# Kernel tuning notes

Measured on AMD Instinct MI355X. Metric: run time of the kernel, lower is better.

## Reference

```python
import jax
import jax.numpy as jnp
import numpy as np

SAMPLE_RATE = 22050
CUTOFF = 0.4 * SAMPLE_RATE  # 0.8 * (sample_rate * 0.5)
Q = 0.707  # torchaudio default


def _biquad_coeffs():
    # torchaudio.functional.lowpass_biquad coefficient formulas
    w0 = 2.0 * np.pi * CUTOFF / SAMPLE_RATE  # = 0.8*pi
    alpha = np.sin(w0) / (2.0 * Q)
    cosw = np.cos(w0)
    a0 = 1.0 + alpha
    b0 = (1.0 - cosw) / 2.0 / a0
    b1 = (1.0 - cosw) / a0
    b2 = b0
    a1 = -2.0 * cosw / a0
    a2 = (1.0 - alpha) / a0
    return np.float32(b0), np.float32(b1), np.float32(b2), np.float32(a1), np.float32(a2)


def setup_inputs() -> dict:
    key = jax.random.key(0)
    inputs = jax.random.normal(key, (64, 262144), dtype=jnp.float32)
    return {"inputs": inputs}


def reference(inputs):
    b0, b1, b2, a1, a2 = _biquad_coeffs()
    x = inputs  # [B, T]
    # FIR (numerator) part, fully parallel
    x1 = jnp.pad(x[:, :-1], ((0, 0), (1, 0)))
    x2 = jnp.pad(x[:, :-2], ((0, 0), (2, 0)))
    u = b0 * x + b1 * x1 + b2 * x2  # [B, T]

    # IIR (denominator) recurrence: y[t] = u[t] - a1*y[t-1] - a2*y[t-2]
    def step(carry, ut):
        y1, y2 = carry
        y = ut - a1 * y1 - a2 * y2
        return (y, y1), y

    z = jnp.zeros(x.shape[0], dtype=x.dtype)
    _, ys = jax.lax.scan(step, (z, z), u.T)  # scan over time, carry [B]
    # torchaudio lfilter clamps output to [-1, 1] by default
    return jnp.clip(ys.T, -1.0, 1.0)
```

## Files before the change

kernel.cpp:

```cpp
#include <hip/hip_runtime.h>
#include <math.h>

constexpr int T_LEN = 262144;
constexpr int CH    = 16;
constexpr int WARM  = 48;
constexpr int TPB   = 256;
constexpr int SEG   = TPB * CH;
constexpr int LTOT  = SEG + WARM;
constexpr int LSWZ  = LTOT + LTOT/16 + 4;
constexpr int BPR   = T_LEN / SEG;

__device__ __forceinline__ int swz(int i) { return i + (i >> 4); }

__global__ __launch_bounds__(TPB, 8) void lowpass_kernel(
    const float* __restrict__ x, float* __restrict__ out,
    float b0, float b1, float b2, float a1, float a2)
{
    __shared__ float lds[LSWZ];
    const int tid = threadIdx.x;
    const size_t rbase = (size_t)(blockIdx.x / BPR) * T_LEN;
    const int blk  = blockIdx.x % BPR;
    const int seg0 = blk * SEG;
    const float* __restrict__ xr = x   + rbase;
    float*       __restrict__ yr = out + rbase;

    for (int m = tid; m < LTOT / 4; m += TPB) {
        const int idx  = 4 * m;
        const int gpos = seg0 - WARM + idx;
        float4 v = make_float4(0.f, 0.f, 0.f, 0.f);
        if (gpos >= 0) v = *reinterpret_cast<const float4*>(xr + gpos);
        const int sb = swz(idx);
        lds[sb + 0] = v.x; lds[sb + 1] = v.y;
        lds[sb + 2] = v.z; lds[sb + 3] = v.w;
    }
    __syncthreads();

    float x1 = 0.f, x2 = 0.f, y1 = 0.f, y2 = 0.f;
    const int b = 17 * tid;
    float o[CH];
    #pragma unroll
    for (int t = 0; t < WARM; ++t) {
        const float xc = lds[b + t + (t >> 4)];
        const float u  = fmaf(b0, xc, fmaf(b1, x1, b2 * x2));
        const float y  = fmaf(-a1, y1, fmaf(-a2, y2, u));
        x2 = x1; x1 = xc; y2 = y1; y1 = y;
    }
    #pragma unroll
    for (int t = 0; t < CH; ++t) {
        const float xc = lds[b + 51 + t];
        const float u  = fmaf(b0, xc, fmaf(b1, x1, b2 * x2));
        const float y  = fmaf(-a1, y1, fmaf(-a2, y2, u));
        x2 = x1; x1 = xc; y2 = y1; y1 = y;
        o[t] = fminf(fmaxf(y, -1.f), 1.f);
    }
    __syncthreads();

    #pragma unroll
    for (int t = 0; t < CH; ++t) lds[b + 51 + t] = o[t];
    __syncthreads();

    for (int m = tid; m < SEG / 4; m += TPB) {
        const int sb = 51 + 4 * m + (m >> 2);
        float4 v = make_float4(lds[sb], lds[sb + 1], lds[sb + 2], lds[sb + 3]);
        *reinterpret_cast<float4*>(yr + seg0 + 4 * m) = v;
    }
}

extern "C" void kernel_launch(void* const* d_in, const int* in_sizes, int n_in,
                              void* d_out, int out_size, void* d_ws, size_t ws_size,
                              hipStream_t stream) {
    const float* x = (const float*)d_in[0];
    float* out = (float*)d_out;
    const int rows = in_sizes[0] / T_LEN;

    const double SR = 22050.0, CUT = 0.4 * SR, Q = 0.707;
    double w0 = 2.0 * M_PI * CUT / SR;
    double alpha = sin(w0) / (2.0 * Q);
    double cosw = cos(w0);
    double a0d = 1.0 + alpha;
    float b0 = (float)((1.0 - cosw) / 2.0 / a0d);
    float b1 = (float)((1.0 - cosw) / a0d);
    float b2 = b0;
    float a1 = (float)(-2.0 * cosw / a0d);
    float a2 = (float)((1.0 - alpha) / a0d);

    const int blocks = rows * BPR;
    lowpass_kernel<<<blocks, TPB, 0, stream>>>(x, out, b0, b1, b2, a1, a2);
}
```

Before: 30.35 us.

## Use XOR-swizzled LDS with float4 accesses and shorten warm-up window

Replaces the padded (i + i/16) shared-memory layout with an XOR swizzle, so global-to-LDS staging, per-thread chunk reads and output writes can all use 128-bit float4 LDS accesses. The per-thread warm-up window is cut from 48 to 24 samples, which reduces redundant recurrence work and staging size. The staging loops are unrolled and the launch-bounds occupancy hint is lowered from 8 to 6. The shorter warm-up relies on the filter's impulse response decaying within 24 samples, which risks accuracy at segment boundaries.

```diff
diff --git a/kernel.cpp b/kernel.cpp
--- a/kernel.cpp
+++ b/kernel.cpp
@@ -3,65 +3,74 @@
 
 constexpr int T_LEN = 262144;
 constexpr int CH    = 16;
-constexpr int WARM  = 48;
+constexpr int WARM  = 24;
 constexpr int TPB   = 256;
 constexpr int SEG   = TPB * CH;
 constexpr int LTOT  = SEG + WARM;
-constexpr int LSWZ  = LTOT + LTOT/16 + 4;
+constexpr int LSWZ  = LTOT + 8;
 constexpr int BPR   = T_LEN / SEG;
 
-__device__ __forceinline__ int swz(int i) { return i + (i >> 4); }
+__device__ __forceinline__ int sw(int i) { return i ^ (((i >> 4) & 7) << 2); }
 
-__global__ __launch_bounds__(TPB, 8) void lowpass_kernel(
+__global__ __launch_bounds__(TPB, 6) void lowpass_kernel(
     const float* __restrict__ x, float* __restrict__ out,
     float b0, float b1, float b2, float a1, float a2)
 {
     __shared__ float lds[LSWZ];
     const int tid = threadIdx.x;
     const size_t rbase = (size_t)(blockIdx.x / BPR) * T_LEN;
-    const int blk  = blockIdx.x % BPR;
-    const int seg0 = blk * SEG;
+    const int seg0 = (blockIdx.x % BPR) * SEG;
     const float* __restrict__ xr = x   + rbase;
     float*       __restrict__ yr = out + rbase;
 
-    for (int m = tid; m < LTOT / 4; m += TPB) {
-        const int idx  = 4 * m;
-        const int gpos = seg0 - WARM + idx;
-        float4 v = make_float4(0.f, 0.f, 0.f, 0.f);
-        if (gpos >= 0) v = *reinterpret_cast<const float4*>(xr + gpos);
-        const int sb = swz(idx);
-        lds[sb + 0] = v.x; lds[sb + 1] = v.y;
-        lds[sb + 2] = v.z; lds[sb + 3] = v.w;
+    #pragma unroll
+    for (int j = 0; j < (LTOT / 4 + TPB - 1) / TPB; ++j) {
+        const int m = tid + j * TPB;
+        if (m < LTOT / 4) {
+            const int idx  = 4 * m;
+            const int gpos = seg0 - WARM + idx;
+            float4 v = make_float4(0.f, 0.f, 0.f, 0.f);
+            if (gpos >= 0) v = *reinterpret_cast<const float4*>(xr + gpos);
+            *reinterpret_cast<float4*>(&lds[sw(idx)]) = v;
+        }
     }
     __syncthreads();
 
     float x1 = 0.f, x2 = 0.f, y1 = 0.f, y2 = 0.f;
-    const int b = 17 * tid;
-    float o[CH];
+    const int base = 16 * tid;
+
+    auto step = [&](float xc) -> float {
+        const float u = fmaf(b0, xc, fmaf(b1, x1, b2 * x2));
+        const float y = fmaf(-a1, y1, fmaf(-a2, y2, u));
+        x2 = x1; x1 = xc; y2 = y1; y1 = y;
+        return y;
+    };
+
     #pragma unroll
-    for (int t = 0; t < WARM; ++t) {
-        const float xc = lds[b + t + (t >> 4)];
-        const float u  = fmaf(b0, xc, fmaf(b1, x1, b2 * x2));
-        const float y  = fmaf(-a1, y1, fmaf(-a2, y2, u));
-        x2 = x1; x1 = xc; y2 = y1; y1 = y;
+    for (int k = 0; k < WARM / 4; ++k) {
+        float4 xv = *reinterpret_cast<const float4*>(&lds[sw(base + 4 * k)]);
+        step(xv.x); step(xv.y); step(xv.z); step(xv.w);
     }
+    float4 ov[CH / 4];
     #pragma unroll
-    for (int t = 0; t < CH; ++t) {
-        const float xc = lds[b + 51 + t];
-        const float u  = fmaf(b0, xc, fmaf(b1, x1, b2 * x2));
-        const float y  = fmaf(-a1, y1, fmaf(-a2, y2, u));
-        x2 = x1; x1 = xc; y2 = y1; y1 = y;
-        o[t] = fminf(fmaxf(y, -1.f), 1.f);
+    for (int k = 0; k < CH / 4; ++k) {
+        float4 xv = *reinterpret_cast<const float4*>(&lds[sw(base + WARM + 4 * k)]);
+        ov[k].x = fminf(fmaxf(step(xv.x), -1.f), 1.f);
+        ov[k].y = fminf(fmaxf(step(xv.y), -1.f), 1.f);
+        ov[k].z = fminf(fmaxf(step(xv.z), -1.f), 1.f);
+        ov[k].w = fminf(fmaxf(step(xv.w), -1.f), 1.f);
     }
     __syncthreads();
 
     #pragma unroll
-    for (int t = 0; t < CH; ++t) lds[b + 51 + t] = o[t];
+    for (int k = 0; k < CH / 4; ++k)
+        *reinterpret_cast<float4*>(&lds[sw(base + WARM + 4 * k)]) = ov[k];
     __syncthreads();
 
-    for (int m = tid; m < SEG / 4; m += TPB) {
-        const int sb = 51 + 4 * m + (m >> 2);
-        float4 v = make_float4(lds[sb], lds[sb + 1], lds[sb + 2], lds[sb + 3]);
+    #pragma unroll
+    for (int j = 0; j < SEG / 4 / TPB; ++j) {
+        const int m = tid + j * TPB;
+        float4 v = *reinterpret_cast<const float4*>(&lds[sw(WARM + 4 * m)]);
         *reinterpret_cast<float4*>(yr + seg0 + 4 * m) = v;
     }
 }
```

Result: faster. 28.10 us (-7.4%).
